# Performance work log

Hardware: AMD Instinct MI355X
Metric: run time of the kernel (lower is better)

Reference implementation:

```python
import jax, jax.numpy as jnp
import numpy as np

N_HEADS = 16
D_KV = 64
NUM_BUCKETS = 64      # bidirectional T5 buckets
MAX_DISTANCE = 50     # hist_step


def _rel_bucket(rel_pos):
    # T5 bidirectional relative-position bucketing.
    nb = NUM_BUCKETS // 2
    ret = (rel_pos > 0).astype(jnp.int32) * nb
    n = jnp.abs(rel_pos)
    max_exact = nb // 2
    is_small = n < max_exact
    large = max_exact + (
        jnp.log(jnp.maximum(n, 1).astype(jnp.float32) / max_exact)
        / np.log(MAX_DISTANCE / max_exact)
        * (nb - max_exact)
    ).astype(jnp.int32)
    large = jnp.minimum(large, nb - 1)
    return ret + jnp.where(is_small, n, large)


def _position_bias(rel_table, qlen, klen):
    ctx = jnp.arange(qlen)[:, None]
    mem = jnp.arange(klen)[None, :]
    bucket = _rel_bucket(mem - ctx)            # (q, k)
    vals = rel_table[bucket]                   # (q, k, h)
    return jnp.transpose(vals, (2, 0, 1))[None]  # (1, h, q, k)


def setup_inputs() -> dict:
    key = jax.random.key(0)
    ks = jax.random.split(key, 11)
    bs, qlen, d_model = 2, 2048, 1024
    inner = N_HEADS * D_KV
    s = 0.02
    return {
        "x": jax.random.normal(ks[0], (bs, qlen, d_model), jnp.float32),
        "Wq": jax.random.normal(ks[1], (d_model, inner), jnp.float32) * s,
        "bq": jnp.zeros((inner,), jnp.float32),
        "Wk": jax.random.normal(ks[2], (d_model, inner), jnp.float32) * s,
        "bk": jnp.zeros((inner,), jnp.float32),
        "Wv": jax.random.normal(ks[3], (d_model, inner), jnp.float32) * s,
        "bv": jnp.zeros((inner,), jnp.float32),
        "Wo": jax.random.normal(ks[4], (inner, d_model), jnp.float32) * s,
        "bo": jnp.zeros((d_model,), jnp.float32),
        "rel_table": jax.random.normal(ks[5], (NUM_BUCKETS, N_HEADS), jnp.float32) * s,
        "mask": jax.random.randint(ks[6], (bs, qlen), 0, 2) > 0,
    }


def reference(x, Wq, bq, Wk, bk, Wv, bv, Wo, bo, rel_table, mask):
    bs, qlen, d_model = x.shape

    def shape(h):  # (b, s, inner) -> (b, n, s, d)
        return h.reshape(bs, qlen, N_HEADS, D_KV).transpose(0, 2, 1, 3)

    q = shape(x @ Wq + bq)
    k = shape(x @ Wk + bk)
    v = shape(x @ Wv + bv)

    # No 1/sqrt(d) scaling in T5.
    scores = jnp.einsum('bnqd,bnkd->bnqk', q, k)

    mask_f = jnp.where(mask, -jnp.inf, 0.0).astype(scores.dtype)[:, None, None, :]  # (b,1,1,k)
    pos_bias = _position_bias(rel_table, qlen, qlen)  # (1,h,q,k)
    add = pos_bias + mask_f                           # bias + mask, broadcast over q

    weights = jax.nn.softmax(scores + add, axis=-1)   # dropout p=0 -> identity
    context = jnp.einsum('bnqk,bnkd->bnqd', weights, v)
    context = context.transpose(0, 2, 1, 3).reshape(bs, qlen, N_HEADS * D_KV)
    out = context @ Wo + bo
    return out, weights, pos_bias
```

## Files before the change

### kernel.cpp

```cpp
#include <hip/hip_runtime.h>
#include <math.h>

typedef _Float16 f16;
typedef f16 f16x8 __attribute__((ext_vector_type(8)));
typedef f16 f16x4 __attribute__((ext_vector_type(4)));
typedef float f32x4 __attribute__((ext_vector_type(4)));

#define W_OFF   (2*2048*1024)
#define PB_OFF  (W_OFF + 2LL*16*2048*2048)

#define NEG_BIG (-1.0e30f)

__device__ __forceinline__ void gload_lds16(const f16* g, f16* l) {
    __builtin_amdgcn_global_load_lds(
        (const __attribute__((address_space(1))) void*)g,
        (__attribute__((address_space(3))) void*)l,
        16, 0, 0);
}

__device__ __forceinline__ int rel_bucket(int rel) {
    int ret = rel > 0 ? 32 : 0;
    int n = rel < 0 ? -rel : rel;
    if (n < 16) return ret + n;
    float fn = (float)n;
    float t = logf(fn * (1.0f / 16.0f));
    t = t / 1.1394343f;
    int large = 16 + (int)(t * 16.0f);
    if (large > 31) large = 31;
    return ret + large;
}


__global__ __launch_bounds__(256)
void conv_f16_kernel(const float* __restrict__ in, f16* __restrict__ out) {
    size_t i = ((size_t)blockIdx.x * 256 + threadIdx.x) * 4;
    float4 v = *(const float4*)&in[i];
    f16x4 h = { (f16)v.x, (f16)v.y, (f16)v.z, (f16)v.w };
    *(f16x4*)&out[i] = h;
}

__global__ __launch_bounds__(256)
void transpose_w_kernel(const float* __restrict__ W, f16* __restrict__ Wt) {
    __shared__ float tile[64 * 68];
    const int tid = threadIdx.x;
    const int bi = blockIdx.x, bj = blockIdx.y;
    #pragma unroll
    for (int it = 0; it < 4; ++it) {
        int slot = tid + it * 256;
        int row = slot >> 4, col4 = (slot & 15) * 4;
        float4 v = *(const float4*)&W[(size_t)(bi * 64 + row) * 1024 + bj * 64 + col4];
        *(float4*)&tile[row * 68 + col4] = v;
    }
    __syncthreads();
    #pragma unroll
    for (int it = 0; it < 4; ++it) {
        int slot = tid + it * 256;
        int nrow = slot >> 4, kcol4 = (slot & 15) * 4;
        f16x4 h;
        #pragma unroll
        for (int j = 0; j < 4; ++j)
            h[j] = (f16)tile[(kcol4 + j) * 68 + nrow];
        *(f16x4*)&Wt[(size_t)(bj * 64 + nrow) * 1024 + bi * 64 + kcol4] = h;
    }
}

__global__ __launch_bounds__(256)
void bias_tbl_kernel(const float* __restrict__ rel_table, float* __restrict__ tbl) {
    int idx = blockIdx.x * 256 + threadIdx.x;
    int h = idx >> 12, dd = idx & 4095;
    tbl[idx] = rel_table[rel_bucket(dd - 2047) * 16 + h];
}

__global__ __launch_bounds__(256)
void concat_bias_kernel(const float* __restrict__ bq, const float* __restrict__ bk,
                        const float* __restrict__ bv, float* __restrict__ o) {
    int i = blockIdx.x * 256 + threadIdx.x;
    float v = i < 1024 ? bq[i] : (i < 2048 ? bk[i - 1024] : bv[i - 2048]);
    o[i] = v;
}

__global__ __launch_bounds__(256)
void transpose_v_kernel(const f16* __restrict__ vh, f16* __restrict__ vt) {
    __shared__ f16 tile[64 * 72];
    const int tid = threadIdx.x;
    const int st = blockIdx.x, bh = blockIdx.y;
    #pragma unroll
    for (int it = 0; it < 2; ++it) {
        int slot = tid + it * 256;
        int row = slot >> 3, col8 = (slot & 7) * 8;
        f16x8 v = *(const f16x8*)&vh[((size_t)bh * 2048 + st * 64 + row) * 64 + col8];
        *(f16x8*)&tile[row * 72 + col8] = v;
    }
    __syncthreads();
    #pragma unroll
    for (int it = 0; it < 2; ++it) {
        int slot = tid + it * 256;
        int drow = slot >> 3, scol8 = (slot & 7) * 8;
        f16x8 r;
        #pragma unroll
        for (int j = 0; j < 8; ++j)
            r[j] = tile[(scol8 + j) * 72 + drow];
        *(f16x8*)&vt[((size_t)bh * 64 + drow) * 2048 + st * 64 + scol8] = r;
    }
}

__global__ __launch_bounds__(256)
void gemm_f16(const f16* __restrict__ A, const f16* __restrict__ Bt,
              const float* __restrict__ bias, void* __restrict__ Cout, int mode)
{
    __shared__ f16 aLDS[128 * 32];
    __shared__ f16 bLDS[128 * 32];
    const int tid = threadIdx.x;
    const int lane = tid & 63, wv = tid >> 6;
    const int quad = lane >> 4, l15 = lane & 15;
    const int wm = (wv & 1) * 64, wn = (wv >> 1) * 64;
    const int bm = blockIdx.y * 128, bn = blockIdx.x * 128;

    f32x4 acc[4][4];
    #pragma unroll
    for (int i = 0; i < 4; ++i)
        #pragma unroll
        for (int j = 0; j < 4; ++j)
            acc[i][j] = (f32x4){0.f, 0.f, 0.f, 0.f};

    for (int k0 = 0; k0 < 1024; k0 += 32) {
        __syncthreads();
        #pragma unroll
        for (int s = 0; s < 2; ++s) {
            int row = (wv + s * 4) * 16 + l15;
            gload_lds16(&A [(size_t)(bm + row) * 1024 + k0 + quad * 8],
                        &aLDS[(size_t)(s * 256 + wv * 64) * 8]);
            gload_lds16(&Bt[(size_t)(bn + row) * 1024 + k0 + quad * 8],
                        &bLDS[(size_t)(s * 256 + wv * 64) * 8]);
        }
        __syncthreads();
        f16x8 af[4], bf[4];
        #pragma unroll
        for (int i = 0; i < 4; ++i) {
            af[i] = *(const f16x8*)&aLDS[(((wm >> 4) + i) * 64 + lane) * 8];
            bf[i] = *(const f16x8*)&bLDS[(((wn >> 4) + i) * 64 + lane) * 8];
        }
        #pragma unroll
        for (int i = 0; i < 4; ++i)
            #pragma unroll
            for (int j = 0; j < 4; ++j)
                acc[i][j] = __builtin_amdgcn_mfma_f32_16x16x32_f16(af[i], bf[j], acc[i][j], 0, 0, 0);
    }

    #pragma unroll
    for (int j = 0; j < 4; ++j) {
        int n = bn + wn + j * 16 + l15;
        float bz = bias[n];
        #pragma unroll
        for (int i = 0; i < 4; ++i) {
            #pragma unroll
            for (int r = 0; r < 4; ++r) {
                int m = bm + wm + i * 16 + quad * 4 + r;
                float val = acc[i][j][r] + bz;
                if (mode == 0) {
                    ((float*)Cout)[(size_t)m * 1024 + n] = val;
                } else {
                    int b = m >> 11, srow = m & 2047;
                    int buf = n >> 10, h = (n >> 6) & 15, d = n & 63;
                    ((f16*)Cout)[(size_t)buf * 4194304 +
                                 (((size_t)(b * 16 + h) * 2048 + srow) << 6) + d] = (f16)val;
                }
            }
        }
    }
}

__global__ __launch_bounds__(256)
void attn_f16(const f16* __restrict__ qh, const f16* __restrict__ kh,
              const f16* __restrict__ vth, const float* __restrict__ tbl,
              const int* __restrict__ mask, float* __restrict__ wout,
              f16* __restrict__ ctxh)
{
    __shared__ float biasL[4096];
    __shared__ float maskL[2048];
    __shared__ f16 wnat[4 * 16 * 88];

    const int tid = threadIdx.x, lane = tid & 63, wv = tid >> 6;
    const int quad = lane >> 4, l15 = lane & 15;

    const int lin = blockIdx.y * 32 + blockIdx.x;
    const int nl = (lin & 7) * 128 + (lin >> 3);
    const int bh = nl >> 5, b = bh >> 4, h = bh & 15;
    const int qt0 = (nl & 31) * 64;

    for (int i = tid; i < 1024; i += 256)
        *(float4*)&biasL[i * 4] = *(const float4*)&tbl[h * 4096 + i * 4];
    for (int i = tid; i < 512; i += 256) {
        int4 mv = *(const int4*)&mask[b * 2048 + i * 4];
        float4 f;
        f.x = mv.x ? NEG_BIG : -20.f;  f.y = mv.y ? NEG_BIG : -20.f;
        f.z = mv.z ? NEG_BIG : -20.f;  f.w = mv.w ? NEG_BIG : -20.f;
        *(float4*)&maskL[i * 4] = f;
    }

    const int q0 = qt0 + wv * 16;
    f16x8 aq[2];
    #pragma unroll
    for (int ds = 0; ds < 2; ++ds)
        aq[ds] = *(const f16x8*)&qh[((size_t)bh * 2048 + q0 + l15) * 64 + ds * 32 + quad * 8];
    __syncthreads();

    const int qrow_base = q0 + quad * 4;
    const f16* kB = kh  + (size_t)bh * 2048 * 64 + quad * 8;
    const f16* vB = vth + (size_t)bh * 64 * 2048 + quad * 8;

    float lI[4] = {0.f, 0.f, 0.f, 0.f};

    for (int c = 0; c < 32; ++c) {
        f16x8 bf[2][4];
        #pragma unroll
        for (int nt = 0; nt < 4; ++nt) {
            const f16* kp = kB + (size_t)(c * 64 + nt * 16 + l15) * 64;
            bf[0][nt] = *(const f16x8*)&kp[0];
            bf[1][nt] = *(const f16x8*)&kp[32];
        }
        #pragma unroll
        for (int nt = 0; nt < 4; ++nt) {
            f32x4 s4 = (f32x4){0.f, 0.f, 0.f, 0.f};
            s4 = __builtin_amdgcn_mfma_f32_16x16x32_f16(aq[0], bf[0][nt], s4, 0, 0, 0);
            s4 = __builtin_amdgcn_mfma_f32_16x16x32_f16(aq[1], bf[1][nt], s4, 0, 0, 0);
            int k = c * 64 + nt * 16 + l15;
            float mk = maskL[k];
            int bi = k - qrow_base + 2047;
            #pragma unroll
            for (int r = 0; r < 4; ++r)
                lI[r] += __expf(s4[r] + biasL[bi - r] + mk);
        }
    }
    #pragma unroll
    for (int r = 0; r < 4; ++r) {
        float l = lI[r];
        l += __shfl_xor(l, 1, 64);
        l += __shfl_xor(l, 2, 64);
        l += __shfl_xor(l, 4, 64);
        l += __shfl_xor(l, 8, 64);
        lI[r] = 1.0f / l;
    }

    float* wbase = wout + (size_t)bh * 2048 * 2048;
    f32x4 oacc[4];
    #pragma unroll
    for (int nt = 0; nt < 4; ++nt) oacc[nt] = (f32x4){0.f, 0.f, 0.f, 0.f};

    for (int c = 0; c < 32; ++c) {
        f16x8 bf[2][4];
        #pragma unroll
        for (int nt = 0; nt < 4; ++nt) {
            const f16* kp = kB + (size_t)(c * 64 + nt * 16 + l15) * 64;
            bf[0][nt] = *(const f16x8*)&kp[0];
            bf[1][nt] = *(const f16x8*)&kp[32];
        }
        f16x8 vf[2][4];
        #pragma unroll
        for (int nt = 0; nt < 4; ++nt) {
            const f16* vp = vB + (size_t)(nt * 16 + l15) * 2048 + c * 64;
            vf[0][nt] = *(const f16x8*)&vp[0];
            vf[1][nt] = *(const f16x8*)&vp[32];
        }

        #pragma unroll
        for (int nt = 0; nt < 4; ++nt) {
            f32x4 s4 = (f32x4){0.f, 0.f, 0.f, 0.f};
            s4 = __builtin_amdgcn_mfma_f32_16x16x32_f16(aq[0], bf[0][nt], s4, 0, 0, 0);
            s4 = __builtin_amdgcn_mfma_f32_16x16x32_f16(aq[1], bf[1][nt], s4, 0, 0, 0);
            int k = c * 64 + nt * 16 + l15;
            float mk = maskL[k];
            int bi = k - qrow_base + 2047;
            float* wp = wbase + (size_t)qrow_base * 2048 + k;
            #pragma unroll
            for (int r = 0; r < 4; ++r) {
                float w = __expf(s4[r] + biasL[bi - r] + mk) * lI[r];
                wp[(size_t)r * 2048] = w;
                wnat[wv * 1408 + (quad * 4 + r) * 88 + nt * 16 + l15] = (f16)w;
            }
        }
        #pragma unroll
        for (int ks = 0; ks < 2; ++ks) {
            f16x8 wf = *(const f16x8*)&wnat[wv * 1408 + l15 * 88 + ks * 32 + quad * 8];
            #pragma unroll
            for (int nt = 0; nt < 4; ++nt)
                oacc[nt] = __builtin_amdgcn_mfma_f32_16x16x32_f16(wf, vf[ks][nt], oacc[nt], 0, 0, 0);
        }
    }

    #pragma unroll
    for (int nt = 0; nt < 4; ++nt) {
        int d = nt * 16 + l15;
        #pragma unroll
        for (int r = 0; r < 4; ++r) {
            int q = qrow_base + r;
            ctxh[((size_t)(b * 2048) + q) * 1024 + h * 64 + d] = (f16)oacc[nt][r];
        }
    }
}

__global__ __launch_bounds__(256)
void posbias_kernel(const float* __restrict__ rel_table, float* __restrict__ pb)
{
    size_t g = ((size_t)blockIdx.x * 256 + threadIdx.x) * 4;
    int k = (int)(g & 2047);
    int q = (int)((g >> 11) & 2047);
    int h = (int)(g >> 22);
    float4 r;
    float* rp = (float*)&r;
    #pragma unroll
    for (int j = 0; j < 4; ++j)
        rp[j] = rel_table[rel_bucket(k + j - q) * 16 + h];
    *(float4*)&pb[g] = r;
}

extern "C" void kernel_launch(void* const* d_in, const int* in_sizes, int n_in,
                              void* d_out, int out_size, void* d_ws, size_t ws_size,
                              hipStream_t stream) {
    const float* x    = (const float*)d_in[0];
    const float* Wq   = (const float*)d_in[1];
    const float* bq   = (const float*)d_in[2];
    const float* Wk   = (const float*)d_in[3];
    const float* bk   = (const float*)d_in[4];
    const float* Wv   = (const float*)d_in[5];
    const float* bv   = (const float*)d_in[6];
    const float* Wo   = (const float*)d_in[7];
    const float* bo   = (const float*)d_in[8];
    const float* rt   = (const float*)d_in[9];
    const int*   mask = (const int*)d_in[10];

    float* out = (float*)d_out;
    float* wts = out + W_OFF;
    float* pb  = out + PB_OFF;

    float* tbl  = pb;
    f16*   xh   = (f16*)(pb + 65536);
    f16*   wqt  = (f16*)(pb + 2162688);
    f16*   wkt  = (f16*)(pb + 2686976);
    f16*   wvt  = (f16*)(pb + 3211264);
    f16*   wot  = (f16*)(pb + 3735552);
    f16*   qh   = (f16*)(pb + 4259840);
    f16*   kh   = (f16*)(pb + 6356992);
    f16*   vh   = (f16*)(pb + 8454144);
    f16*   vth  = (f16*)(pb + 10551296);
    f16*   ctxh = (f16*)(pb + 12648448);
    float* bqkv = pb + 14745600;

    dim3 blk(256);
    conv_f16_kernel<<<dim3(4096), blk, 0, stream>>>(x, xh);
    transpose_w_kernel<<<dim3(16, 16), blk, 0, stream>>>(Wq, wqt);
    transpose_w_kernel<<<dim3(16, 16), blk, 0, stream>>>(Wk, wkt);
    transpose_w_kernel<<<dim3(16, 16), blk, 0, stream>>>(Wv, wvt);
    transpose_w_kernel<<<dim3(16, 16), blk, 0, stream>>>(Wo, wot);
    bias_tbl_kernel<<<dim3(256), blk, 0, stream>>>(rt, tbl);
    concat_bias_kernel<<<dim3(12), blk, 0, stream>>>(bq, bk, bv, bqkv);

    gemm_f16<<<dim3(24, 32), blk, 0, stream>>>(xh, wqt, bqkv, qh, 1);
    transpose_v_kernel<<<dim3(32, 32), blk, 0, stream>>>(vh, vth);

    attn_f16<<<dim3(32, 32), blk, 0, stream>>>(qh, kh, vth, tbl, mask, wts, ctxh);

    gemm_f16<<<dim3(8, 32), blk, 0, stream>>>(ctxh, wot, bo, out, 0);
    posbias_kernel<<<dim3(65536), blk, 0, stream>>>(rt, pb);
}
```

Baseline: 1.259 ms.

## Stage K/V tiles in LDS via global_load_lds and use table lookup for posbias

```diff
diff --git a/kernel.cpp b/kernel.cpp
--- a/kernel.cpp
+++ b/kernel.cpp
@@ -178,6 +178,8 @@
 {
     __shared__ float biasL[4096];
     __shared__ float maskL[2048];
+    __shared__ f16 kL[8 * 64 * 8];
+    __shared__ f16 vL[8 * 64 * 8];
     __shared__ f16 wnat[4 * 16 * 88];
 
     const int tid = threadIdx.x, lane = tid & 63, wv = tid >> 6;
@@ -203,27 +205,31 @@
     #pragma unroll
     for (int ds = 0; ds < 2; ++ds)
         aq[ds] = *(const f16x8*)&qh[((size_t)bh * 2048 + q0 + l15) * 64 + ds * 32 + quad * 8];
-    __syncthreads();
 
     const int qrow_base = q0 + quad * 4;
-    const f16* kB = kh  + (size_t)bh * 2048 * 64 + quad * 8;
-    const f16* vB = vth + (size_t)bh * 64 * 2048 + quad * 8;
+    const f16* kB = kh  + (size_t)bh * 2048 * 64;
+    const f16* vB = vth + (size_t)bh * 64 * 2048;
 
     float lI[4] = {0.f, 0.f, 0.f, 0.f};
 
     for (int c = 0; c < 32; ++c) {
-        f16x8 bf[2][4];
-        #pragma unroll
-        for (int nt = 0; nt < 4; ++nt) {
-            const f16* kp = kB + (size_t)(c * 64 + nt * 16 + l15) * 64;
-            bf[0][nt] = *(const f16x8*)&kp[0];
-            bf[1][nt] = *(const f16x8*)&kp[32];
-        }
+        __syncthreads();
+        #pragma unroll
+        for (int s = 0; s < 2; ++s) {
+            int f = wv + s * 4;
+            int dstep = f >> 2, nt = f & 3;
+            gload_lds16(&kB[(size_t)(c * 64 + nt * 16 + l15) * 64 + dstep * 32 + quad * 8],
+                        &kL[(size_t)(s * 256 + wv * 64) * 8]);
+        }
+        __syncthreads();
         #pragma unroll
         for (int nt = 0; nt < 4; ++nt) {
             f32x4 s4 = (f32x4){0.f, 0.f, 0.f, 0.f};
-            s4 = __builtin_amdgcn_mfma_f32_16x16x32_f16(aq[0], bf[0][nt], s4, 0, 0, 0);
-            s4 = __builtin_amdgcn_mfma_f32_16x16x32_f16(aq[1], bf[1][nt], s4, 0, 0, 0);
+            #pragma unroll
+            for (int ds = 0; ds < 2; ++ds) {
+                f16x8 bf = *(const f16x8*)&kL[((ds * 4 + nt) * 64 + lane) * 8];
+                s4 = __builtin_amdgcn_mfma_f32_16x16x32_f16(aq[ds], bf, s4, 0, 0, 0);
+            }
             int k = c * 64 + nt * 16 + l15;
             float mk = maskL[k];
             int bi = k - qrow_base + 2047;
@@ -248,26 +254,31 @@
     for (int nt = 0; nt < 4; ++nt) oacc[nt] = (f32x4){0.f, 0.f, 0.f, 0.f};
 
     for (int c = 0; c < 32; ++c) {
-        f16x8 bf[2][4];
-        #pragma unroll
-        for (int nt = 0; nt < 4; ++nt) {
-            const f16* kp = kB + (size_t)(c * 64 + nt * 16 + l15) * 64;
-            bf[0][nt] = *(const f16x8*)&kp[0];
-            bf[1][nt] = *(const f16x8*)&kp[32];
-        }
-        f16x8 vf[2][4];
-        #pragma unroll
-        for (int nt = 0; nt < 4; ++nt) {
-            const f16* vp = vB + (size_t)(nt * 16 + l15) * 2048 + c * 64;
-            vf[0][nt] = *(const f16x8*)&vp[0];
-            vf[1][nt] = *(const f16x8*)&vp[32];
-        }
+        __syncthreads();
+        #pragma unroll
+        for (int s = 0; s < 2; ++s) {
+            int f = wv + s * 4;
+            {
+                int dstep = f >> 2, nt = f & 3;
+                gload_lds16(&kB[(size_t)(c * 64 + nt * 16 + l15) * 64 + dstep * 32 + quad * 8],
+                            &kL[(size_t)(s * 256 + wv * 64) * 8]);
+            }
+            {
+                int ks = f >> 2, nt = f & 3;
+                gload_lds16(&vB[(size_t)(nt * 16 + l15) * 2048 + c * 64 + ks * 32 + quad * 8],
+                            &vL[(size_t)(s * 256 + wv * 64) * 8]);
+            }
+        }
+        __syncthreads();
 
         #pragma unroll
         for (int nt = 0; nt < 4; ++nt) {
             f32x4 s4 = (f32x4){0.f, 0.f, 0.f, 0.f};
-            s4 = __builtin_amdgcn_mfma_f32_16x16x32_f16(aq[0], bf[0][nt], s4, 0, 0, 0);
-            s4 = __builtin_amdgcn_mfma_f32_16x16x32_f16(aq[1], bf[1][nt], s4, 0, 0, 0);
+            #pragma unroll
+            for (int ds = 0; ds < 2; ++ds) {
+                f16x8 bf = *(const f16x8*)&kL[((ds * 4 + nt) * 64 + lane) * 8];
+                s4 = __builtin_amdgcn_mfma_f32_16x16x32_f16(aq[ds], bf, s4, 0, 0, 0);
+            }
             int k = c * 64 + nt * 16 + l15;
             float mk = maskL[k];
             int bi = k - qrow_base + 2047;
@@ -283,8 +294,10 @@
         for (int ks = 0; ks < 2; ++ks) {
             f16x8 wf = *(const f16x8*)&wnat[wv * 1408 + l15 * 88 + ks * 32 + quad * 8];
             #pragma unroll
-            for (int nt = 0; nt < 4; ++nt)
-                oacc[nt] = __builtin_amdgcn_mfma_f32_16x16x32_f16(wf, vf[ks][nt], oacc[nt], 0, 0, 0);
+            for (int nt = 0; nt < 4; ++nt) {
+                f16x8 vf = *(const f16x8*)&vL[((ks * 4 + nt) * 64 + lane) * 8];
+                oacc[nt] = __builtin_amdgcn_mfma_f32_16x16x32_f16(wf, vf, oacc[nt], 0, 0, 0);
+            }
         }
     }
 
@@ -311,6 +324,18 @@
     #pragma unroll
     for (int j = 0; j < 4; ++j)
         rp[j] = rel_table[rel_bucket(k + j - q) * 16 + h];
+    *(float4*)&pb[g] = r;
+}
+
+__global__ __launch_bounds__(256)
+void posbias_tbl_kernel(const float* __restrict__ tblw, float* __restrict__ pb)
+{
+    size_t g = ((size_t)blockIdx.x * 256 + threadIdx.x) * 4;
+    int k = (int)(g & 2047);
+    int q = (int)((g >> 11) & 2047);
+    int h = (int)(g >> 22);
+    const float* tp = tblw + h * 4096 + (k - q + 2047);
+    float4 r = { tp[0], tp[1], tp[2], tp[3] };
     *(float4*)&pb[g] = r;
 }
 
@@ -346,6 +371,9 @@
     f16*   ctxh = (f16*)(pb + 12648448);
     float* bqkv = pb + 14745600;
 
+    const bool use_ws = ws_size >= 65536 * sizeof(float);
+    float* tblw = (float*)d_ws;
+
     dim3 blk(256);
     conv_f16_kernel<<<dim3(4096), blk, 0, stream>>>(x, xh);
     transpose_w_kernel<<<dim3(16, 16), blk, 0, stream>>>(Wq, wqt);
@@ -353,6 +381,8 @@
     transpose_w_kernel<<<dim3(16, 16), blk, 0, stream>>>(Wv, wvt);
     transpose_w_kernel<<<dim3(16, 16), blk, 0, stream>>>(Wo, wot);
     bias_tbl_kernel<<<dim3(256), blk, 0, stream>>>(rt, tbl);
+    if (use_ws)
+        bias_tbl_kernel<<<dim3(256), blk, 0, stream>>>(rt, tblw);
     concat_bias_kernel<<<dim3(12), blk, 0, stream>>>(bq, bk, bv, bqkv);
 
     gemm_f16<<<dim3(24, 32), blk, 0, stream>>>(xh, wqt, bqkv, qh, 1);
@@ -361,5 +391,9 @@
     attn_f16<<<dim3(32, 32), blk, 0, stream>>>(qh, kh, vth, tbl, mask, wts, ctxh);
 
     gemm_f16<<<dim3(8, 32), blk, 0, stream>>>(ctxh, wot, bo, out, 0);
-    posbias_kernel<<<dim3(65536), blk, 0, stream>>>(rt, pb);
-}
+
+    if (use_ws)
+        posbias_tbl_kernel<<<dim3(65536), blk, 0, stream>>>(tblw, pb);
+    else
+        posbias_kernel<<<dim3(65536), blk, 0, stream>>>(rt, pb);
+}
```

After: 1.115 ms. -11.4%, faster.
